# Optimization experiments

Measured on AMD Instinct MI355X. Metric: run time of the kernel, lower is better.

The kernel has to match this reference:

```python
import jax, jax.numpy as jnp
import numpy as np

N_NODES = 500_000
DIM_IN = 128
DIM_OUT = 128
N_DISTRICTS = 1024


def setup_inputs() -> dict:
    key = jax.random.key(0)
    k_x, k_z, k_w1, k_w2 = jax.random.split(key, 4)
    x = jax.random.normal(k_x, (N_NODES, DIM_IN), dtype=jnp.float32)
    zone_lst = jax.random.randint(k_z, (N_NODES,), 0, N_DISTRICTS, dtype=jnp.int64)
    # MLP params: Linear(dim_in, 2*dim_in), Linear(2*dim_in, dim_out)
    w1 = jax.random.normal(k_w1, (DIM_IN, 2 * DIM_IN), dtype=jnp.float32) * (1.0 / np.sqrt(DIM_IN))
    b1 = jnp.zeros((2 * DIM_IN,), dtype=jnp.float32)
    w2 = jax.random.normal(k_w2, (2 * DIM_IN, DIM_OUT), dtype=jnp.float32) * (1.0 / np.sqrt(2 * DIM_IN))
    b2 = jnp.zeros((DIM_OUT,), dtype=jnp.float32)
    return {"x": x, "zone_lst": zone_lst, "w1": w1, "b1": b1, "w2": w2, "b2": b2}


def reference(x, zone_lst, w1, b1, w2, b2):
    # Per-district sum of node features: one fused segment reduction
    # (replaces the python loop over districts in the original).
    head = jax.ops.segment_sum(x, zone_lst, num_segments=N_DISTRICTS)  # [D, dim_in]
    # MLP: ReLU -> Linear -> ReLU -> Linear
    h = jnp.maximum(head, 0.0)
    h = jnp.maximum(h @ w1 + b1, 0.0)
    return h @ w2 + b2
```

## Files before the change

kernel.cpp:

```cpp
#include <hip/hip_runtime.h>

#define DIM_IN 128
#define DIM_HID 256
#define DIM_OUT 128
#define N_DIST 1024
#define NB 256


__device__ __forceinline__ int detect_is64(const int* __restrict__ zone_raw,
                                           int t, int* s_flag) {
    if (t < 64) {
        bool hi_zero = (zone_raw[2 * t + 1] == 0);
        unsigned long long m = __ballot(hi_zero);
        if (t == 0) *s_flag = (m == ~0ull) ? 1 : 0;
    }
    __syncthreads();
    return *s_flag;
}

__global__ __launch_bounds__(256)
void hist_kernel(const int* __restrict__ zone, int n,
                 int* __restrict__ blockHist) {
    __shared__ int lhist[N_DIST];
    __shared__ int s_is64;
    const int t = threadIdx.x;
    const int b = blockIdx.x;
    for (int i = t; i < N_DIST; i += 256) lhist[i] = 0;
    const int is64 = detect_is64(zone, t, &s_is64);

    const int chunk = (n + NB - 1) / NB;
    const int start = b * chunk;
    const int end = min(n, start + chunk);
    const long long* zone64 = (const long long*)zone;
    for (int i = start + t; i < end; i += 256) {
        int z = is64 ? (int)zone64[i] : zone[i];
        atomicAdd(&lhist[z], 1);
    }
    __syncthreads();
    for (int i = t; i < N_DIST; i += 256) blockHist[b * N_DIST + i] = lhist[i];
}

__global__ __launch_bounds__(1024)
void scan_kernel(int* __restrict__ blockHist,
                 int* __restrict__ offsets, int* __restrict__ counts) {
    __shared__ int tmp[N_DIST];
    const int d = threadIdx.x;
    int c = 0;
#pragma unroll 8
    for (int b = 0; b < NB; b++) c += blockHist[b * N_DIST + d];
    counts[d] = c;
    tmp[d] = c;
    __syncthreads();
    for (int off = 1; off < N_DIST; off <<= 1) {
        int add = (d >= off) ? tmp[d - off] : 0;
        __syncthreads();
        tmp[d] += add;
        __syncthreads();
    }
    const int excl = tmp[d] - c;
    offsets[d] = excl;
    int run = excl;
    for (int b = 0; b < NB; b++) {
        int v = blockHist[b * N_DIST + d];
        blockHist[b * N_DIST + d] = run;
        run += v;
    }
}

__global__ __launch_bounds__(256)
void scatter_kernel(const int* __restrict__ zone, int n,
                    const int* __restrict__ blockStart,
                    int* __restrict__ sorted) {
    __shared__ int lcur[N_DIST];
    __shared__ int s_is64;
    const int t = threadIdx.x;
    const int b = blockIdx.x;
    for (int i = t; i < N_DIST; i += 256) lcur[i] = blockStart[b * N_DIST + i];
    const int is64 = detect_is64(zone, t, &s_is64);

    const int chunk = (n + NB - 1) / NB;
    const int start = b * chunk;
    const int end = min(n, start + chunk);
    const long long* zone64 = (const long long*)zone;
    for (int i = start + t; i < end; i += 256) {
        int z = is64 ? (int)zone64[i] : zone[i];
        int pos = atomicAdd(&lcur[z], 1);
        sorted[pos] = i;
    }
}

__global__ __launch_bounds__(256)
void district_kernel(const float* __restrict__ x, const int* __restrict__ sorted,
                     const int* __restrict__ offsets, const int* __restrict__ counts,
                     const float* __restrict__ w1, const float* __restrict__ b1,
                     const float* __restrict__ w2, const float* __restrict__ b2,
                     float* __restrict__ out) {
    const int d = blockIdx.x;
    const int start = offsets[d];
    const int cnt = counts[d];
    const int t = threadIdx.x;
    const int q = t & 31;
    const int g = t >> 5;

    const float* xq = x + (size_t)q * 4;
    float4 a0 = make_float4(0.f, 0.f, 0.f, 0.f);
    float4 a1 = a0, a2 = a0, a3 = a0;

    int n = g;
    for (; n + 24 < cnt; n += 32) {
        int i0 = sorted[start + n];
        int i1 = sorted[start + n + 8];
        int i2 = sorted[start + n + 16];
        int i3 = sorted[start + n + 24];
        float4 v0 = *(const float4*)(xq + (size_t)i0 * DIM_IN);
        float4 v1 = *(const float4*)(xq + (size_t)i1 * DIM_IN);
        float4 v2 = *(const float4*)(xq + (size_t)i2 * DIM_IN);
        float4 v3 = *(const float4*)(xq + (size_t)i3 * DIM_IN);
        a0.x += v0.x; a0.y += v0.y; a0.z += v0.z; a0.w += v0.w;
        a1.x += v1.x; a1.y += v1.y; a1.z += v1.z; a1.w += v1.w;
        a2.x += v2.x; a2.y += v2.y; a2.z += v2.z; a2.w += v2.w;
        a3.x += v3.x; a3.y += v3.y; a3.z += v3.z; a3.w += v3.w;
    }
    for (; n < cnt; n += 8) {
        int i0 = sorted[start + n];
        float4 v0 = *(const float4*)(xq + (size_t)i0 * DIM_IN);
        a0.x += v0.x; a0.y += v0.y; a0.z += v0.z; a0.w += v0.w;
    }
    a0.x += a1.x + a2.x + a3.x;
    a0.y += a1.y + a2.y + a3.y;
    a0.z += a1.z + a2.z + a3.z;
    a0.w += a1.w + a2.w + a3.w;

    __shared__ float part[8][DIM_IN];
    part[g][q * 4 + 0] = a0.x;
    part[g][q * 4 + 1] = a0.y;
    part[g][q * 4 + 2] = a0.z;
    part[g][q * 4 + 3] = a0.w;
    __syncthreads();

    __shared__ float hrelu[DIM_IN];
    if (t < DIM_IN) {
        float s = 0.f;
#pragma unroll
        for (int gg = 0; gg < 8; gg++) s += part[gg][t];
        hrelu[t] = fmaxf(s, 0.f);
    }
    __syncthreads();

    float s1 = b1[t];
#pragma unroll 8
    for (int k = 0; k < DIM_IN; k++) {
        s1 = fmaf(hrelu[k], w1[k * DIM_HID + t], s1);
    }
    __shared__ float h1[DIM_HID];
    h1[t] = fmaxf(s1, 0.f);
    __syncthreads();

    if (t < DIM_OUT) {
        float s2 = b2[t];
#pragma unroll 8
        for (int j = 0; j < DIM_HID; j++) {
            s2 = fmaf(h1[j], w2[j * DIM_OUT + t], s2);
        }
        out[d * DIM_OUT + t] = s2;
    }
}

extern "C" void kernel_launch(void* const* d_in, const int* in_sizes, int n_in,
                              void* d_out, int out_size, void* d_ws, size_t ws_size,
                              hipStream_t stream) {
    const float* x    = (const float*)d_in[0];
    const int*   zone = (const int*)d_in[1];
    const float* w1   = (const float*)d_in[2];
    const float* b1   = (const float*)d_in[3];
    const float* w2   = (const float*)d_in[4];
    const float* b2   = (const float*)d_in[5];
    float* out = (float*)d_out;
    const int n = in_sizes[0] / DIM_IN;

    char* ws = (char*)d_ws;
    int* counts    = (int*)(ws);
    int* offsets   = (int*)(ws + 4096);
    int* blockHist = (int*)(ws + 65536);
    int* sorted    = (int*)(ws + (2u << 20));

    hist_kernel<<<NB, 256, 0, stream>>>(zone, n, blockHist);
    scan_kernel<<<1, N_DIST, 0, stream>>>(blockHist, offsets, counts);
    scatter_kernel<<<NB, 256, 0, stream>>>(zone, n, blockHist, sorted);
    district_kernel<<<N_DIST, 256, 0, stream>>>(x, sorted, offsets, counts,
                                                w1, b1, w2, b2, out);
}
```

Measured before the change: 407.3 us.

## Parallelize block-histogram scan across blocks and stage sorted indices in LDS

```diff
diff --git a/kernel.cpp b/kernel.cpp
--- a/kernel.cpp
+++ b/kernel.cpp
@@ -40,15 +40,41 @@
     for (int i = t; i < N_DIST; i += 256) blockHist[b * N_DIST + i] = lhist[i];
 }
 
+__global__ __launch_bounds__(256)
+void scanA_kernel(int* __restrict__ blockHist, int* __restrict__ counts) {
+    const int t = threadIdx.x;
+    const int lane = t & 63;
+    const int w = t >> 6;
+    const int d = blockIdx.x * 4 + w;
+
+    int v0 = blockHist[(4 * lane + 0) * N_DIST + d];
+    int v1 = blockHist[(4 * lane + 1) * N_DIST + d];
+    int v2 = blockHist[(4 * lane + 2) * N_DIST + d];
+    int v3 = blockHist[(4 * lane + 3) * N_DIST + d];
+    const int tsum = v0 + v1 + v2 + v3;
+
+    int s = tsum;
+#pragma unroll
+    for (int off = 1; off < 64; off <<= 1) {
+        int u = __shfl_up(s, off);
+        if (lane >= off) s += u;
+    }
+    const int total = __shfl(s, 63);
+    int excl = s - tsum;
+
+    blockHist[(4 * lane + 0) * N_DIST + d] = excl; excl += v0;
+    blockHist[(4 * lane + 1) * N_DIST + d] = excl; excl += v1;
+    blockHist[(4 * lane + 2) * N_DIST + d] = excl; excl += v2;
+    blockHist[(4 * lane + 3) * N_DIST + d] = excl;
+
+    if (lane == 0) counts[d] = total;
+}
+
 __global__ __launch_bounds__(1024)
-void scan_kernel(int* __restrict__ blockHist,
-                 int* __restrict__ offsets, int* __restrict__ counts) {
+void scanB_kernel(const int* __restrict__ counts, int* __restrict__ offsets) {
     __shared__ int tmp[N_DIST];
     const int d = threadIdx.x;
-    int c = 0;
-#pragma unroll 8
-    for (int b = 0; b < NB; b++) c += blockHist[b * N_DIST + d];
-    counts[d] = c;
+    const int c = counts[d];
     tmp[d] = c;
     __syncthreads();
     for (int off = 1; off < N_DIST; off <<= 1) {
@@ -57,25 +83,20 @@
         tmp[d] += add;
         __syncthreads();
     }
-    const int excl = tmp[d] - c;
-    offsets[d] = excl;
-    int run = excl;
-    for (int b = 0; b < NB; b++) {
-        int v = blockHist[b * N_DIST + d];
-        blockHist[b * N_DIST + d] = run;
-        run += v;
-    }
+    offsets[d] = tmp[d] - c;
 }
 
 __global__ __launch_bounds__(256)
 void scatter_kernel(const int* __restrict__ zone, int n,
                     const int* __restrict__ blockStart,
+                    const int* __restrict__ offsets,
                     int* __restrict__ sorted) {
     __shared__ int lcur[N_DIST];
     __shared__ int s_is64;
     const int t = threadIdx.x;
     const int b = blockIdx.x;
-    for (int i = t; i < N_DIST; i += 256) lcur[i] = blockStart[b * N_DIST + i];
+    for (int i = t; i < N_DIST; i += 256)
+        lcur[i] = offsets[i] + blockStart[b * N_DIST + i];
     const int is64 = detect_is64(zone, t, &s_is64);
 
     const int chunk = (n + NB - 1) / NB;
@@ -102,30 +123,40 @@
     const int q = t & 31;
     const int g = t >> 5;
 
+    __shared__ int sidx[1024];
+
     const float* xq = x + (size_t)q * 4;
     float4 a0 = make_float4(0.f, 0.f, 0.f, 0.f);
     float4 a1 = a0, a2 = a0, a3 = a0;
 
-    int n = g;
-    for (; n + 24 < cnt; n += 32) {
-        int i0 = sorted[start + n];
-        int i1 = sorted[start + n + 8];
-        int i2 = sorted[start + n + 16];
-        int i3 = sorted[start + n + 24];
-        float4 v0 = *(const float4*)(xq + (size_t)i0 * DIM_IN);
-        float4 v1 = *(const float4*)(xq + (size_t)i1 * DIM_IN);
-        float4 v2 = *(const float4*)(xq + (size_t)i2 * DIM_IN);
-        float4 v3 = *(const float4*)(xq + (size_t)i3 * DIM_IN);
-        a0.x += v0.x; a0.y += v0.y; a0.z += v0.z; a0.w += v0.w;
-        a1.x += v1.x; a1.y += v1.y; a1.z += v1.z; a1.w += v1.w;
-        a2.x += v2.x; a2.y += v2.y; a2.z += v2.z; a2.w += v2.w;
-        a3.x += v3.x; a3.y += v3.y; a3.z += v3.z; a3.w += v3.w;
-    }
-    for (; n < cnt; n += 8) {
-        int i0 = sorted[start + n];
-        float4 v0 = *(const float4*)(xq + (size_t)i0 * DIM_IN);
-        a0.x += v0.x; a0.y += v0.y; a0.z += v0.z; a0.w += v0.w;
-    }
+    for (int base = 0; base < cnt; base += 1024) {
+        const int m = min(cnt - base, 1024);
+        for (int i = t; i < m; i += 256) sidx[i] = sorted[start + base + i];
+        __syncthreads();
+
+        int n = g;
+        for (; n + 24 < m; n += 32) {
+            int i0 = sidx[n];
+            int i1 = sidx[n + 8];
+            int i2 = sidx[n + 16];
+            int i3 = sidx[n + 24];
+            float4 v0 = *(const float4*)(xq + (size_t)i0 * DIM_IN);
+            float4 v1 = *(const float4*)(xq + (size_t)i1 * DIM_IN);
+            float4 v2 = *(const float4*)(xq + (size_t)i2 * DIM_IN);
+            float4 v3 = *(const float4*)(xq + (size_t)i3 * DIM_IN);
+            a0.x += v0.x; a0.y += v0.y; a0.z += v0.z; a0.w += v0.w;
+            a1.x += v1.x; a1.y += v1.y; a1.z += v1.z; a1.w += v1.w;
+            a2.x += v2.x; a2.y += v2.y; a2.z += v2.z; a2.w += v2.w;
+            a3.x += v3.x; a3.y += v3.y; a3.z += v3.z; a3.w += v3.w;
+        }
+        for (; n < m; n += 8) {
+            int i0 = sidx[n];
+            float4 v0 = *(const float4*)(xq + (size_t)i0 * DIM_IN);
+            a0.x += v0.x; a0.y += v0.y; a0.z += v0.z; a0.w += v0.w;
+        }
+        __syncthreads();
+    }
+
     a0.x += a1.x + a2.x + a3.x;
     a0.y += a1.y + a2.y + a3.y;
     a0.z += a1.z + a2.z + a3.z;
@@ -185,8 +216,9 @@
     int* sorted    = (int*)(ws + (2u << 20));
 
     hist_kernel<<<NB, 256, 0, stream>>>(zone, n, blockHist);
-    scan_kernel<<<1, N_DIST, 0, stream>>>(blockHist, offsets, counts);
-    scatter_kernel<<<NB, 256, 0, stream>>>(zone, n, blockHist, sorted);
+    scanA_kernel<<<N_DIST / 4, 256, 0, stream>>>(blockHist, counts);
+    scanB_kernel<<<1, N_DIST, 0, stream>>>(counts, offsets);
+    scatter_kernel<<<NB, 256, 0, stream>>>(zone, n, blockHist, offsets, sorted);
     district_kernel<<<N_DIST, 256, 0, stream>>>(x, sorted, offsets, counts,
                                                 w1, b1, w2, b2, out);
 }
```

New measurement: 388.4 us. 1.05x faster.
